# Kernel optimization log

Hardware: AMD Instinct MI355X
Metric: run time of the kernel (lower is better)

Reference implementation:

```python
import jax, jax.numpy as jnp
import numpy as np
import math

DIM = 2048
NUM_HEADS = 32
HEAD_DIM = DIM // NUM_HEADS  # 64; HEAD_DIM//2 == NUM_HEADS (required by original rope broadcasting)
SEQ_LEN = 2048
BATCH = 2
ROPE_BASE = 10000.0


def apply_rope(inputs, positions):
    # Faithful to original: positions is [L]; sinusoid broadcasts to [1, L, H/2, 1]
    # and then multiplies [B, L, N, H/2] -- the original code relies on N == H/2.
    head_dim = inputs.shape[-1]
    fraction = 2.0 * jnp.arange(head_dim // 2, dtype=inputs.dtype) / head_dim
    timescale = ROPE_BASE ** fraction                      # [H/2]
    sinusoid = positions[:, None] / timescale[None, None, :]  # [1, L, H/2]
    sinusoid = sinusoid[..., None]                         # [1, L, H/2, 1]
    sin = jnp.sin(sinusoid)
    cos = jnp.cos(sinusoid)
    first, second = jnp.split(inputs, 2, axis=-1)          # each [B, L, N, H/2]
    return jnp.concatenate([first * cos - second * sin,
                            second * cos + first * sin], axis=-1)


def setup_inputs() -> dict:
    key = jax.random.key(0)
    ks = jax.random.split(key, 9)
    s = 0.02
    inp = {
        'x': jax.random.normal(ks[0], (BATCH, SEQ_LEN, DIM), dtype=jnp.float32),
        'wq_w': jax.random.normal(ks[1], (DIM, DIM), dtype=jnp.float32) * s,
        'wq_b': jnp.zeros((DIM,), dtype=jnp.float32),
        'wk_w': jax.random.normal(ks[2], (DIM, DIM), dtype=jnp.float32) * s,
        'wk_b': jnp.zeros((DIM,), dtype=jnp.float32),
        'wv_w': jax.random.normal(ks[3], (DIM, DIM), dtype=jnp.float32) * s,
        'wv_b': jnp.zeros((DIM,), dtype=jnp.float32),
        'wo_w': jax.random.normal(ks[4], (DIM, DIM), dtype=jnp.float32) * s,
        'wo_b': jnp.zeros((DIM,), dtype=jnp.float32),
    }
    return inp


def reference(x, wq_w, wq_b, wk_w, wk_b, wv_w, wv_b, wo_w, wo_b):
    B, L, _ = x.shape
    N, H = NUM_HEADS, HEAD_DIM
    q = (x @ wq_w.T + wq_b).reshape(B, L, N, H)
    k = (x @ wk_w.T + wk_b).reshape(B, L, N, H)
    v = (x @ wv_w.T + wv_b).reshape(B, L, N, H)
    positions = jnp.arange(L, dtype=x.dtype)
    q = apply_rope(q, positions)
    k = apply_rope(k, positions)
    # [B, N, L, H]
    q = q.transpose(0, 2, 1, 3)
    k = k.transpose(0, 2, 1, 3)
    v = v.transpose(0, 2, 1, 3)
    scale = math.sqrt(H)
    scores = jnp.einsum('bnqh,bnkh->bnqk', q, k) / scale   # [B, N, L, L]
    causal = jnp.tril(jnp.ones((L, L), dtype=bool))
    scores = jnp.where(causal[None, None], scores, -jnp.inf)
    attn = jax.nn.softmax(scores, axis=-1)
    context = jnp.einsum('bnqk,bnkh->bnqh', attn, v)        # [B, N, L, H]
    context = context.transpose(0, 2, 1, 3).reshape(B, L, DIM)
    return context @ wo_w.T + wo_b
```

## Files before the change

### kernel.cpp

```cpp
#include <hip/hip_runtime.h>
#include <stdint.h>

#define D_MODEL 2048
#define SEQLEN  2048

typedef float f32x4  __attribute__((ext_vector_type(4)));
typedef float f32x16 __attribute__((ext_vector_type(16)));
typedef int   i32x4  __attribute__((ext_vector_type(4)));
typedef short s16x4  __attribute__((ext_vector_type(4)));
typedef __bf16 bf16x8 __attribute__((ext_vector_type(8)));

__device__ __forceinline__ unsigned short f2bf(float f) {
  union { float f; uint32_t u; } x; x.f = f;
  uint32_t r = (x.u + 0x7FFFu + ((x.u >> 16) & 1u)) >> 16;
  return (unsigned short)r;
}

__device__ __forceinline__ bf16x8 as_bf16x8(i32x4 v) {
  union { i32x4 i; bf16x8 b; } u; u.i = v; return u.b;
}

#define MFMA16(acc, a, b) \
  acc = __builtin_amdgcn_mfma_f32_16x16x32_bf16(as_bf16x8(a), as_bf16x8(b), acc, 0, 0, 0)
#define MFMA32(acc, a, b) \
  acc = __builtin_amdgcn_mfma_f32_32x32x16_bf16(as_bf16x8(a), as_bf16x8(b), acc, 0, 0, 0)

__device__ __forceinline__ void gload16(const void* g, void* lds) {
  __builtin_amdgcn_global_load_lds(
      (const __attribute__((address_space(1))) unsigned int*)(uintptr_t)g,
      (__attribute__((address_space(3))) unsigned int*)(uint32_t)(uintptr_t)lds,
      16, 0, 0);
}

__global__ void cvt_bf16_k(const float* __restrict__ in,
                           unsigned short* __restrict__ out, int n4) {
  int i = blockIdx.x * 256 + threadIdx.x;
  if (i < n4) {
    f32x4 v = *(const f32x4*)&in[(size_t)i * 4];
    s16x4 o;
#pragma unroll
    for (int j = 0; j < 4; ++j) o[j] = (short)f2bf(v[j]);
    *(s16x4*)&out[(size_t)i * 4] = o;
  }
}

template <bool ROPE, bool F32OUT>
__global__ __launch_bounds__(256) void gemm_nt(
    const unsigned short* __restrict__ A, const unsigned short* __restrict__ B,
    const float* __restrict__ bias, unsigned short* __restrict__ Cb,
    float* __restrict__ Cf) {
  __shared__ alignas(16) unsigned short As[128 * 64];
  __shared__ alignas(16) unsigned short Bs[128 * 64];

  const int t = threadIdx.x;
  const int w = t >> 6, l = t & 63;
  const int wm = w >> 1, wn = w & 1;
  const int band = l >> 4, ln = l & 15;
  const int m0 = blockIdx.y * 128, n0 = blockIdx.x * 128;

  f32x4 acc[4][4] = {};

  const int srow = t >> 3;
  const int scol = (t & 7) * 8;
  const unsigned short* Ab = A + (size_t)(m0 + srow) * D_MODEL + scol;
  const unsigned short* Bb = B + (size_t)(n0 + srow) * D_MODEL + scol;

  for (int kt = 0; kt < D_MODEL / 64; ++kt) {
    const int k0 = kt * 64;
#pragma unroll
    for (int i = 0; i < 4; ++i) {
      gload16(Ab + i * 32 * D_MODEL + k0, &As[(i * 4 + w) * 512]);
      gload16(Bb + i * 32 * D_MODEL + k0, &Bs[(i * 4 + w) * 512]);
    }
    __syncthreads();
#pragma unroll
    for (int kk = 0; kk < 2; ++kk) {
      i32x4 av[4], bv[4];
#pragma unroll
      for (int mf = 0; mf < 4; ++mf)
        av[mf] = *(const i32x4*)&As[(wm * 64 + mf * 16 + ln) * 64 + kk * 32 + band * 8];
#pragma unroll
      for (int nf = 0; nf < 4; ++nf)
        bv[nf] = *(const i32x4*)&Bs[(wn * 64 + nf * 16 + ln) * 64 + kk * 32 + band * 8];
#pragma unroll
      for (int mf = 0; mf < 4; ++mf)
#pragma unroll
        for (int nf = 0; nf < 4; ++nf)
          MFMA16(acc[mf][nf], av[mf], bv[nf]);
    }
    __syncthreads();
  }

  float bb[4];
#pragma unroll
  for (int nf = 0; nf < 4; ++nf) bb[nf] = bias[n0 + wn * 64 + nf * 16 + ln];
#pragma unroll
  for (int mf = 0; mf < 4; ++mf)
#pragma unroll
    for (int nf = 0; nf < 4; ++nf)
#pragma unroll
      for (int r = 0; r < 4; ++r) acc[mf][nf][r] += bb[nf];

  if constexpr (ROPE) {
    const int head = (n0 + wn * 64) >> 6;
    const float ts = powf(10000.0f, (float)head * (1.0f / 32.0f));
#pragma unroll
    for (int mf = 0; mf < 4; ++mf) {
#pragma unroll
      for (int r = 0; r < 4; ++r) {
        const int row = m0 + wm * 64 + mf * 16 + band * 4 + r;
        const float pos = (float)(row & (SEQLEN - 1));
        float sv, cv;
        sincosf(pos / ts, &sv, &cv);
#pragma unroll
        for (int p = 0; p < 2; ++p) {
          const float f0 = acc[mf][p][r], s0 = acc[mf][p + 2][r];
          acc[mf][p][r]     = f0 * cv - s0 * sv;
          acc[mf][p + 2][r] = s0 * cv + f0 * sv;
        }
      }
    }
  }

#pragma unroll
  for (int mf = 0; mf < 4; ++mf)
#pragma unroll
    for (int nf = 0; nf < 4; ++nf)
#pragma unroll
      for (int r = 0; r < 4; ++r) {
        const size_t row = m0 + wm * 64 + mf * 16 + band * 4 + r;
        const int col = n0 + wn * 64 + nf * 16 + ln;
        if constexpr (F32OUT) Cf[row * D_MODEL + col] = acc[mf][nf][r];
        else                  Cb[row * D_MODEL + col] = f2bf(acc[mf][nf][r]);
      }
}

__global__ __launch_bounds__(256) void attn_fwd(
    const unsigned short* __restrict__ Q, const unsigned short* __restrict__ K,
    const unsigned short* __restrict__ V, unsigned short* __restrict__ O) {
  __shared__ alignas(16) unsigned short Ks[64 * 64];
  __shared__ alignas(16) unsigned short Vt[64 * 80];

  const int t = threadIdx.x;
  const int w = t >> 6, l = t & 63;
  const int l31 = l & 31, t5 = l >> 5;
  const int bx = blockIdx.x, head = blockIdx.y, b = blockIdx.z;
  const int h0 = head * 64;
  const size_t rb = (size_t)b * SEQLEN;

  const int vg = t & 7, vrow = t >> 3;
  const int kdr = l >> 3, kdb = l & 7;

  for (int pi = 0; pi < 2; ++pi) {
    const int qt = pi ? (15 - bx) : bx;
    const int q0 = qt * 128;
    const int qg = q0 + w * 32 + l31;

    i32x4 qf[4];
#pragma unroll
    for (int hk = 0; hk < 4; ++hk)
      qf[hk] = *(const i32x4*)&Q[(rb + qg) * D_MODEL + h0 + hk * 16 + t5 * 8];

    f32x16 oacc[2] = {};
    float lsum = 0.f;

    const int nkt = qt * 2 + 2;
    for (int kt = 0; kt < nkt; ++kt) {
      const int k0 = kt * 64;
#pragma unroll
      for (int i = 0; i < 2; ++i) {
        const int drow = (i * 4 + w) * 8 + kdr;
        const int sblk = kdb ^ (drow & 7);
        gload16(&K[(rb + k0 + drow) * D_MODEL + h0 + sblk * 8], &Ks[(i * 4 + w) * 512]);
      }
#pragma unroll
      for (int i = 0; i < 2; ++i) {
        const int r = i * 32 + vrow, c8 = vg * 8;
        i32x4 vv = *(const i32x4*)&V[(rb + k0 + r) * D_MODEL + h0 + c8];
        union { i32x4 v; unsigned short s[8]; } u; u.v = vv;
#pragma unroll
        for (int j = 0; j < 8; ++j) Vt[(c8 + j) * 80 + (r ^ c8)] = u.s[j];
      }
      __syncthreads();

      f32x16 sacc[2] = {};
#pragma unroll
      for (int kvf = 0; kvf < 2; ++kvf) {
        const int krow = kvf * 32 + l31;
#pragma unroll
        for (int hk = 0; hk < 4; ++hk) {
          i32x4 a = *(const i32x4*)&Ks[krow * 64 + ((2 * hk + t5) ^ (krow & 7)) * 8];
          MFMA32(sacc[kvf], a, qf[hk]);
        }
      }

      const bool needmask = (k0 + 64 > q0 + w * 32);
      uint32_t W[2][4][2];
#pragma unroll
      for (int kvf = 0; kvf < 2; ++kvf)
#pragma unroll
        for (int g = 0; g < 4; ++g)
#pragma unroll
          for (int p = 0; p < 2; ++p) {
            uint32_t wd = 0;
#pragma unroll
            for (int e = 0; e < 2; ++e) {
              const int reg = 4 * g + 2 * p + e;
              const int kvl = kvf * 32 + 8 * g + 4 * t5 + 2 * p + e;
              float pv = __expf(sacc[kvf][reg] * 0.125f);
              if (needmask && (k0 + kvl > qg)) pv = 0.f;
              lsum += pv;
              wd |= (uint32_t)f2bf(pv) << (16 * e);
            }
            W[kvf][g][p] = wd;
          }

#pragma unroll
      for (int ks = 0; ks < 4; ++ks) {
        const int kvf = ks >> 1;
        const int gA = 2 * (ks & 1), gB = gA + 1;
        const uint32_t O0 = t5 ? W[kvf][gB][0] : W[kvf][gA][0];
        const uint32_t O1 = t5 ? W[kvf][gB][1] : W[kvf][gA][1];
        const uint32_t E0 = t5 ? W[kvf][gA][0] : W[kvf][gB][0];
        const uint32_t E1 = t5 ? W[kvf][gA][1] : W[kvf][gB][1];
        const uint32_t X0 = (uint32_t)__shfl_xor((int)E0, 32);
        const uint32_t X1 = (uint32_t)__shfl_xor((int)E1, 32);
        i32x4 pf;
        pf[0] = (int)(t5 ? X0 : O0);
        pf[1] = (int)(t5 ? X1 : O1);
        pf[2] = (int)(t5 ? O0 : X0);
        pf[3] = (int)(t5 ? O1 : X1);
#pragma unroll
        for (int hf = 0; hf < 2; ++hf) {
          const int h = hf * 32 + l31;
          i32x4 vb = *(const i32x4*)&Vt[h * 80 + ((ks * 16 + t5 * 8) ^ ((h >> 3) * 8))];
          MFMA32(oacc[hf], pf, vb);
        }
      }
      __syncthreads();
    }

    lsum += __shfl_xor(lsum, 32);
    const float inv = 1.0f / lsum;

#pragma unroll
    for (int g2 = 0; g2 < 4; ++g2)
#pragma unroll
      for (int rr = 0; rr < 4; ++rr) {
        const int rowl = rr + 8 * g2 + 4 * t5;
        const float invr = __shfl(inv, (l & 32) + rowl);
        const size_t gr = rb + q0 + w * 32 + rowl;
#pragma unroll
        for (int hf = 0; hf < 2; ++hf)
          O[gr * D_MODEL + h0 + hf * 32 + l31] = f2bf(oacc[hf][4 * g2 + rr] * invr);
      }
  }
}

extern "C" void kernel_launch(void* const* d_in, const int* in_sizes, int n_in,
                              void* d_out, int out_size, void* d_ws, size_t ws_size,
                              hipStream_t stream) {
  const float* x    = (const float*)d_in[0];
  const float* wq_w = (const float*)d_in[1];
  const float* wq_b = (const float*)d_in[2];
  const float* wk_w = (const float*)d_in[3];
  const float* wk_b = (const float*)d_in[4];
  const float* wv_w = (const float*)d_in[5];
  const float* wv_b = (const float*)d_in[6];
  const float* wo_w = (const float*)d_in[7];
  const float* wo_b = (const float*)d_in[8];
  float* out = (float*)d_out;

  unsigned short* ws  = (unsigned short*)d_ws;
  unsigned short* xb  = ws;
  unsigned short* wqb = xb  + 8388608;
  unsigned short* wkb = wqb + 4194304;
  unsigned short* wvb = wkb + 4194304;
  unsigned short* wob = wvb + 4194304;
  unsigned short* qb  = wob + 4194304;
  unsigned short* kb  = qb  + 8388608;
  unsigned short* vb  = kb  + 8388608;
  unsigned short* cb  = xb;

  cvt_bf16_k<<<8192, 256, 0, stream>>>(x, xb, 2097152);
  cvt_bf16_k<<<4096, 256, 0, stream>>>(wq_w, wqb, 1048576);
  cvt_bf16_k<<<4096, 256, 0, stream>>>(wk_w, wkb, 1048576);
  cvt_bf16_k<<<4096, 256, 0, stream>>>(wv_w, wvb, 1048576);
  cvt_bf16_k<<<4096, 256, 0, stream>>>(wo_w, wob, 1048576);

  dim3 g(16, 32);
  gemm_nt<true,  false><<<g, 256, 0, stream>>>(xb, wqb, wq_b, qb, nullptr);
  gemm_nt<true,  false><<<g, 256, 0, stream>>>(xb, wkb, wk_b, kb, nullptr);
  gemm_nt<false, false><<<g, 256, 0, stream>>>(xb, wvb, wv_b, vb, nullptr);

  attn_fwd<<<dim3(8, 32, 2), 256, 0, stream>>>(qb, kb, vb, cb);

  gemm_nt<false, true><<<g, 256, 0, stream>>>(cb, wob, wo_b, nullptr, out);
}
```

Before: 323.4 us.

## Replace GEMMs with double-buffered 256x256 tile kernel and fused QKV launch

Replaces the 128x128 single-buffered GEMM with a 512-thread, 256x256-tile kernel. It double-buffers LDS, prefetches the next k-tile in quarter stages while MFMAs run, and swizzles the LDS layout to avoid bank conflicts. The Q, K and V projections are merged into one launch that picks the weight matrix from blockIdx. The aim is to hide global-load latency, raise data reuse per tile and cut launch overhead. The cost is larger register and LDS use (128KB of LDS per block, so lower occupancy) and fewer blocks for the output projection (128 blocks).

```diff
diff --git a/kernel.cpp b/kernel.cpp
--- a/kernel.cpp
+++ b/kernel.cpp
@@ -44,95 +44,156 @@
   }
 }
 
-template <bool ROPE, bool F32OUT>
-__global__ __launch_bounds__(256) void gemm_nt(
-    const unsigned short* __restrict__ A, const unsigned short* __restrict__ B,
-    const float* __restrict__ bias, unsigned short* __restrict__ Cb,
-    float* __restrict__ Cf) {
-  __shared__ alignas(16) unsigned short As[128 * 64];
-  __shared__ alignas(16) unsigned short Bs[128 * 64];
+template <int MODE>
+__global__ __launch_bounds__(512) void gemm8p(
+    const unsigned short* __restrict__ A,
+    const unsigned short* __restrict__ W0,
+    const unsigned short* __restrict__ W1,
+    const unsigned short* __restrict__ W2,
+    const float* __restrict__ bias0,
+    const float* __restrict__ bias1,
+    const float* __restrict__ bias2,
+    unsigned short* __restrict__ O0,
+    unsigned short* __restrict__ O1,
+    unsigned short* __restrict__ O2,
+    float* __restrict__ Of) {
+  __shared__ alignas(16) unsigned short L[8 * 8192];
 
   const int t = threadIdx.x;
   const int w = t >> 6, l = t & 63;
-  const int wm = w >> 1, wn = w & 1;
+  const int wm = w >> 2, wn = w & 3;
   const int band = l >> 4, ln = l & 15;
-  const int m0 = blockIdx.y * 128, n0 = blockIdx.x * 128;
-
-  f32x4 acc[4][4] = {};
-
-  const int srow = t >> 3;
-  const int scol = (t & 7) * 8;
-  const unsigned short* Ab = A + (size_t)(m0 + srow) * D_MODEL + scol;
-  const unsigned short* Bb = B + (size_t)(n0 + srow) * D_MODEL + scol;
-
-  for (int kt = 0; kt < D_MODEL / 64; ++kt) {
-    const int k0 = kt * 64;
-#pragma unroll
-    for (int i = 0; i < 4; ++i) {
-      gload16(Ab + i * 32 * D_MODEL + k0, &As[(i * 4 + w) * 512]);
-      gload16(Bb + i * 32 * D_MODEL + k0, &Bs[(i * 4 + w) * 512]);
+
+  const int bx = blockIdx.x;
+  const int m0 = blockIdx.y * 256;
+
+  const unsigned short* Wm;
+  const float* bias;
+  int nloc, mat;
+  if constexpr (MODE == 0) {
+    mat = bx >> 3;
+    nloc = (bx & 7) * 256;
+    Wm = mat == 0 ? W0 : (mat == 1 ? W1 : W2);
+    bias = mat == 0 ? bias0 : (mat == 1 ? bias1 : bias2);
+  } else {
+    mat = 0;
+    nloc = bx * 256;
+    Wm = W0;
+    bias = bias0;
+  }
+
+  auto stage = [&](int p, int ktile, unsigned short* buf) {
+    const unsigned short* src = (p & 1) ? Wm : A;
+    const int grow0 = (p & 1) ? nloc : m0;
+    unsigned short* dst = buf + ((p & 1) ? 16384 : 0) + (p >> 1) * 8192;
+    const int kcol = ktile * 64 + (p >> 1) * 32;
+#pragma unroll
+    for (int i = 0; i < 2; ++i) {
+      const int pos = (w * 2 + i) * 64 + l;
+      const int row = pos >> 2, blk = pos & 3;
+      const int gblk = blk ^ (row & 3);
+      gload16(&src[(size_t)(grow0 + row) * D_MODEL + kcol + gblk * 8],
+              dst + (w * 2 + i) * 512);
     }
-    __syncthreads();
-#pragma unroll
-    for (int kk = 0; kk < 2; ++kk) {
-      i32x4 av[4], bv[4];
-#pragma unroll
-      for (int mf = 0; mf < 4; ++mf)
-        av[mf] = *(const i32x4*)&As[(wm * 64 + mf * 16 + ln) * 64 + kk * 32 + band * 8];
-#pragma unroll
-      for (int nf = 0; nf < 4; ++nf)
-        bv[nf] = *(const i32x4*)&Bs[(wn * 64 + nf * 16 + ln) * 64 + kk * 32 + band * 8];
-#pragma unroll
-      for (int mf = 0; mf < 4; ++mf)
+  };
+
+  f32x4 acc[8][4] = {};
+
+  stage(0, 0, L);
+  stage(1, 0, L);
+  stage(2, 0, L);
+  stage(3, 0, L);
+  asm volatile("s_waitcnt vmcnt(4)" ::: "memory");
+  __builtin_amdgcn_s_barrier();
+
+  const int arow = wm * 128;
+  for (int kt = 0; kt < 32; ++kt) {
+    unsigned short* Lb = L + (kt & 1) * 32768;
+    unsigned short* Ln = L + ((kt & 1) ^ 1) * 32768;
+    const int ktn = (kt + 1) & 31;
+    i32x4 bv[4];
+#pragma unroll
+    for (int kh = 0; kh < 2; ++kh) {
+      const unsigned short* Apl = Lb + kh * 8192;
+      const unsigned short* Bpl = Lb + 16384 + kh * 8192;
+#pragma unroll
+      for (int hf = 0; hf < 2; ++hf) {
+        i32x4 av[4];
+#pragma unroll
+        for (int mf = 0; mf < 4; ++mf) {
+          const int row = arow + (hf * 4 + mf) * 16 + ln;
+          av[mf] = *(const i32x4*)&Apl[row * 32 + ((band ^ (row & 3)) << 3)];
+        }
+        if (hf == 0) {
+#pragma unroll
+          for (int nf = 0; nf < 4; ++nf) {
+            const int row = wn * 64 + nf * 16 + ln;
+            bv[nf] = *(const i32x4*)&Bpl[row * 32 + ((band ^ (row & 3)) << 3)];
+          }
+        }
+        stage(kh * 2 + hf, ktn, Ln);
+        __builtin_amdgcn_s_barrier();
+        asm volatile("s_waitcnt lgkmcnt(0)" ::: "memory");
+        __builtin_amdgcn_sched_barrier(0);
+        __builtin_amdgcn_s_setprio(1);
+#pragma unroll
+        for (int mf = 0; mf < 4; ++mf)
+#pragma unroll
+          for (int nf = 0; nf < 4; ++nf)
+            MFMA16(acc[hf * 4 + mf][nf], av[mf], bv[nf]);
+        __builtin_amdgcn_s_setprio(0);
+        if (hf == 1) asm volatile("s_waitcnt vmcnt(4)" ::: "memory");
+        __builtin_amdgcn_s_barrier();
+      }
+    }
+  }
+  asm volatile("s_waitcnt vmcnt(0)" ::: "memory");
+
+  float bb[4];
+#pragma unroll
+  for (int nf = 0; nf < 4; ++nf) bb[nf] = bias[nloc + wn * 64 + nf * 16 + ln];
+
+  if constexpr (MODE == 0) {
+    unsigned short* Out = mat == 0 ? O0 : (mat == 1 ? O1 : O2);
+    const bool rope = (mat < 2);
+    const int head = (nloc + wn * 64) >> 6;
+    const float ts = powf(10000.0f, (float)head * (1.0f / 32.0f));
+#pragma unroll
+    for (int am = 0; am < 8; ++am) {
+#pragma unroll
+      for (int r = 0; r < 4; ++r) {
+        const int row = m0 + wm * 128 + am * 16 + band * 4 + r;
+        float vals[4];
+#pragma unroll
+        for (int nf = 0; nf < 4; ++nf) vals[nf] = acc[am][nf][r] + bb[nf];
+        if (rope) {
+          const float pos = (float)(row & (SEQLEN - 1));
+          float sv, cv;
+          sincosf(pos / ts, &sv, &cv);
+#pragma unroll
+          for (int p = 0; p < 2; ++p) {
+            const float f0 = vals[p], s0 = vals[p + 2];
+            vals[p]     = f0 * cv - s0 * sv;
+            vals[p + 2] = s0 * cv + f0 * sv;
+          }
+        }
 #pragma unroll
         for (int nf = 0; nf < 4; ++nf)
-          MFMA16(acc[mf][nf], av[mf], bv[nf]);
+          Out[(size_t)row * D_MODEL + nloc + wn * 64 + nf * 16 + ln] = f2bf(vals[nf]);
+      }
     }
-    __syncthreads();
-  }
-
-  float bb[4];
-#pragma unroll
-  for (int nf = 0; nf < 4; ++nf) bb[nf] = bias[n0 + wn * 64 + nf * 16 + ln];
-#pragma unroll
-  for (int mf = 0; mf < 4; ++mf)
-#pragma unroll
-    for (int nf = 0; nf < 4; ++nf)
-#pragma unroll
-      for (int r = 0; r < 4; ++r) acc[mf][nf][r] += bb[nf];
-
-  if constexpr (ROPE) {
-    const int head = (n0 + wn * 64) >> 6;
-    const float ts = powf(10000.0f, (float)head * (1.0f / 32.0f));
-#pragma unroll
-    for (int mf = 0; mf < 4; ++mf) {
+  } else {
+#pragma unroll
+    for (int am = 0; am < 8; ++am)
 #pragma unroll
       for (int r = 0; r < 4; ++r) {
-        const int row = m0 + wm * 64 + mf * 16 + band * 4 + r;
-        const float pos = (float)(row & (SEQLEN - 1));
-        float sv, cv;
-        sincosf(pos / ts, &sv, &cv);
-#pragma unroll
-        for (int p = 0; p < 2; ++p) {
-          const float f0 = acc[mf][p][r], s0 = acc[mf][p + 2][r];
-          acc[mf][p][r]     = f0 * cv - s0 * sv;
-          acc[mf][p + 2][r] = s0 * cv + f0 * sv;
-        }
-      }
-    }
-  }
-
-#pragma unroll
-  for (int mf = 0; mf < 4; ++mf)
-#pragma unroll
-    for (int nf = 0; nf < 4; ++nf)
-#pragma unroll
-      for (int r = 0; r < 4; ++r) {
-        const size_t row = m0 + wm * 64 + mf * 16 + band * 4 + r;
-        const int col = n0 + wn * 64 + nf * 16 + ln;
-        if constexpr (F32OUT) Cf[row * D_MODEL + col] = acc[mf][nf][r];
-        else                  Cb[row * D_MODEL + col] = f2bf(acc[mf][nf][r]);
-      }
+        const int row = m0 + wm * 128 + am * 16 + band * 4 + r;
+#pragma unroll
+        for (int nf = 0; nf < 4; ++nf)
+          Of[(size_t)row * D_MODEL + nloc + wn * 64 + nf * 16 + ln] =
+              acc[am][nf][r] + bb[nf];
+      }
+  }
 }
 
 __global__ __launch_bounds__(256) void attn_fwd(
@@ -288,12 +349,11 @@
   cvt_bf16_k<<<4096, 256, 0, stream>>>(wv_w, wvb, 1048576);
   cvt_bf16_k<<<4096, 256, 0, stream>>>(wo_w, wob, 1048576);
 
-  dim3 g(16, 32);
-  gemm_nt<true,  false><<<g, 256, 0, stream>>>(xb, wqb, wq_b, qb, nullptr);
-  gemm_nt<true,  false><<<g, 256, 0, stream>>>(xb, wkb, wk_b, kb, nullptr);
-  gemm_nt<false, false><<<g, 256, 0, stream>>>(xb, wvb, wv_b, vb, nullptr);
+  gemm8p<0><<<dim3(24, 16), 512, 0, stream>>>(xb, wqb, wkb, wvb, wq_b, wk_b, wv_b,
+                                              qb, kb, vb, nullptr);
 
   attn_fwd<<<dim3(8, 32, 2), 256, 0, stream>>>(qb, kb, vb, cb);
 
-  gemm_nt<false, true><<<g, 256, 0, stream>>>(cb, wob, wo_b, nullptr, out);
-}
+  gemm8p<1><<<dim3(8, 16), 512, 0, stream>>>(cb, wob, nullptr, nullptr, wo_b, nullptr,
+                                             nullptr, nullptr, nullptr, nullptr, out);
+}
```

Result: faster. 313.7 us (-3.0%).
